# Performance work log

Hardware: AMD Instinct MI355X
Metric: run time of the kernel (lower is better)

The kernel has to match this reference:

```python
import jax, jax.numpy as jnp
import numpy as np

# --- physics constants (from source) ---
T_STALL = 5.4 * (1.0 / 100.0)
W_FREE = 1620.0 * (1.0 / 60.0) * 2.0 * np.pi
L_X = 0.129907
L_Y = 0.095724
A = L_X + L_Y
R = 4 * 0.0254
MASS = 6.0
INERTIA = MASS
MOMENT_OF_INERTIA = MASS * (12 * 0.0254) ** 2 / 6.0

LV2WV = np.array([[1, -1, -A], [1, 1, A], [1, 1, -A], [1, -1, A]], dtype=np.float32) / R  # [4,3]
CD2MD = np.array([[1, -1, -1], [1, 1, 1], [1, 1, -1], [1, -1, 1]], dtype=np.float32)      # [4,3]
WT2LA = (LV2WV.T / np.array([INERTIA, INERTIA, MOMENT_OF_INERTIA], dtype=np.float32)[:, None]).astype(np.float32)  # [3,4]

BATCH = 4_000_000


def _rot(c, s):
    # builds [..., 3, 3] = [[c,-s,0],[s,c,0],[0,0,1]]
    z = jnp.zeros_like(c)
    o = jnp.ones_like(c)
    return jnp.stack([
        jnp.stack([c, -s, z], axis=-1),
        jnp.stack([s, c, z], axis=-1),
        jnp.stack([z, z, o], axis=-1),
    ], axis=-2)


def setup_inputs() -> dict:
    key = jax.random.key(0)
    k1, k2 = jax.random.split(key)
    state = jax.random.normal(k1, (BATCH, 6), dtype=jnp.float32)
    control_duty = jax.random.normal(k2, (3,), dtype=jnp.float32)
    t = jnp.zeros((1,), dtype=jnp.float32)
    return {"t": t, "state": state, "control_duty": control_duty}


def reference(t, state, control_duty):
    lv2wv = jnp.asarray(LV2WV)
    cd2md = jnp.asarray(CD2MD)
    wt2la = jnp.asarray(WT2LA)

    absolute_vel = state[..., 3:]            # [..., 3]
    theta = state[..., 2]                    # [...]

    # absolute -> local frame
    a2l = _rot(jnp.cos(-theta), jnp.sin(-theta))                      # [...,3,3]
    local_vel = jnp.einsum('...ij,...j->...i', a2l, absolute_vel)     # [...,3]
    wheel_vel = jnp.einsum('ij,...j->...i', lv2wv, local_vel)         # [...,4]

    motor_duty = cd2md @ control_duty                                 # [4]
    is_same_direction = (jnp.sign(motor_duty * wheel_vel) + 1.0) / 2.0
    wheel_torque = T_STALL * (1.0 - jnp.abs(wheel_vel) * is_same_direction / W_FREE) * motor_duty  # [...,4]

    local_accel = jnp.einsum('ij,...j->...i', wt2la, wheel_torque)    # [...,3]

    # local -> absolute frame
    l2a = _rot(jnp.cos(theta), jnp.sin(theta))
    absolute_accel = jnp.einsum('...ij,...j->...i', l2a, local_accel)

    return jnp.concatenate([absolute_vel, absolute_accel], axis=-1)   # [...,6]
```

## Files before the change

### kernel.cpp

```cpp
#include <hip/hip_runtime.h>
#include <math.h>

namespace k {
constexpr double dA     = 0.129907 + 0.095724;
constexpr double dR     = 4.0 * 0.0254;
constexpr double dI     = 6.0;
constexpr double dMOI   = 6.0 * (12.0 * 0.0254) * (12.0 * 0.0254) / 6.0;
constexpr float T_STALL   = (float)(5.4 / 100.0);
constexpr float INV_WFREE = (float)(1.0 / (1620.0 / 60.0 * 2.0 * 3.14159265358979323846));
constexpr float A         = (float)dA;
constexpr float INV_R     = (float)(1.0 / dR);
constexpr float INV_RI    = (float)(1.0 / (dR * dI));
constexpr float A_RMOI    = (float)(dA / (dR * dMOI));
}

__device__ __forceinline__ float wheel_torque(float w, float m) {
    float p = m * w;
    float sgn = (float)(p > 0.0f) - (float)(p < 0.0f);
    float isd = 0.5f * (sgn + 1.0f);
    return k::T_STALL * (1.0f - fabsf(w) * isd * k::INV_WFREE) * m;
}

__device__ __forceinline__ void mecanum_elem(const float st[6],
                                             float m0, float m1, float m2, float m3,
                                             float o[6]) {
    float theta = st[2];
    float s, c;
    sincosf(theta, &s, &c);

    float v0 = st[3], v1 = st[4], v2 = st[5];

    float lv0 = c * v0 + s * v1;
    float lv1 = c * v1 - s * v0;
    float lv2 = v2;

    float al2 = k::A * lv2;
    float w0 = (lv0 - lv1 - al2) * k::INV_R;
    float w1 = (lv0 + lv1 + al2) * k::INV_R;
    float w2 = (lv0 + lv1 - al2) * k::INV_R;
    float w3 = (lv0 - lv1 + al2) * k::INV_R;

    float t0 = wheel_torque(w0, m0);
    float t1 = wheel_torque(w1, m1);
    float t2 = wheel_torque(w2, m2);
    float t3 = wheel_torque(w3, m3);

    float la0 = (t0 + t1 + t2 + t3) * k::INV_RI;
    float la1 = (-t0 + t1 + t2 - t3) * k::INV_RI;
    float la2 = (-t0 + t1 - t2 + t3) * k::A_RMOI;

    float aa0 = c * la0 - s * la1;
    float aa1 = s * la0 + c * la1;

    o[0] = v0; o[1] = v1; o[2] = v2;
    o[3] = aa0; o[4] = aa1; o[5] = la2;
}

__global__ __launch_bounds__(256) void mecanum_pair_kernel(
    const float4* __restrict__ state4,
    const float* __restrict__ cd,
    float4* __restrict__ out4,
    int n_pairs) {
    int i = blockIdx.x * blockDim.x + threadIdx.x;
    if (i >= n_pairs) return;

    float u0 = cd[0], u1 = cd[1], u2 = cd[2];
    float m0 = u0 - u1 - u2;
    float m1 = u0 + u1 + u2;
    float m2 = u0 + u1 - u2;
    float m3 = u0 - u1 + u2;

    float4 a = state4[3 * i + 0];
    float4 b = state4[3 * i + 1];
    float4 g = state4[3 * i + 2];

    float stA[6] = { a.x, a.y, a.z, a.w, b.x, b.y };
    float stB[6] = { b.z, b.w, g.x, g.y, g.z, g.w };
    float oA[6], oB[6];
    mecanum_elem(stA, m0, m1, m2, m3, oA);
    mecanum_elem(stB, m0, m1, m2, m3, oB);

    float4 r0 = { oA[0], oA[1], oA[2], oA[3] };
    float4 r1 = { oA[4], oA[5], oB[0], oB[1] };
    float4 r2 = { oB[2], oB[3], oB[4], oB[5] };
    out4[3 * i + 0] = r0;
    out4[3 * i + 1] = r1;
    out4[3 * i + 2] = r2;
}

__global__ void mecanum_tail_kernel(const float* __restrict__ state,
                                    const float* __restrict__ cd,
                                    float* __restrict__ out,
                                    int start, int n) {
    int i = start + blockIdx.x * blockDim.x + threadIdx.x;
    if (i >= n) return;
    float u0 = cd[0], u1 = cd[1], u2 = cd[2];
    float m0 = u0 - u1 - u2;
    float m1 = u0 + u1 + u2;
    float m2 = u0 + u1 - u2;
    float m3 = u0 - u1 + u2;
    float st[6], o[6];
#pragma unroll
    for (int j = 0; j < 6; ++j) st[j] = state[6 * i + j];
    mecanum_elem(st, m0, m1, m2, m3, o);
#pragma unroll
    for (int j = 0; j < 6; ++j) out[6 * i + j] = o[j];
}

extern "C" void kernel_launch(void* const* d_in, const int* in_sizes, int n_in,
                              void* d_out, int out_size, void* d_ws, size_t ws_size,
                              hipStream_t stream) {
    const float* state = (const float*)d_in[1];
    const float* cd    = (const float*)d_in[2];
    float* out         = (float*)d_out;

    int n = in_sizes[1] / 6;
    int n_pairs = n / 2;

    if (n_pairs > 0) {
        int block = 256;
        int grid = (n_pairs + block - 1) / block;
        mecanum_pair_kernel<<<grid, block, 0, stream>>>(
            (const float4*)state, cd, (float4*)out, n_pairs);
    }
    if (n & 1) {
        mecanum_tail_kernel<<<1, 64, 0, stream>>>(state, cd, out, 2 * n_pairs, n);
    }
}
```

Before: 180.7 us.

## Stage state loads and output stores through LDS for fully coalesced access

```diff
diff --git a/kernel.cpp b/kernel.cpp
--- a/kernel.cpp
+++ b/kernel.cpp
@@ -32,9 +32,8 @@
 
     float lv0 = c * v0 + s * v1;
     float lv1 = c * v1 - s * v0;
-    float lv2 = v2;
 
-    float al2 = k::A * lv2;
+    float al2 = k::A * v2;
     float w0 = (lv0 - lv1 - al2) * k::INV_R;
     float w1 = (lv0 + lv1 + al2) * k::INV_R;
     float w2 = (lv0 + lv1 - al2) * k::INV_R;
@@ -52,17 +51,31 @@
     float aa0 = c * la0 - s * la1;
     float aa1 = s * la0 + c * la1;
 
-    o[0] = v0; o[1] = v1; o[2] = v2;
+    o[0] = st[3]; o[1] = st[4]; o[2] = st[5];
     o[3] = aa0; o[4] = aa1; o[5] = la2;
 }
 
-__global__ __launch_bounds__(256) void mecanum_pair_kernel(
+#define PAIRS_PER_BLOCK 256
+#define F4_PER_BLOCK    (PAIRS_PER_BLOCK * 3)
+
+__global__ __launch_bounds__(256) void mecanum_lds_kernel(
     const float4* __restrict__ state4,
     const float* __restrict__ cd,
     float4* __restrict__ out4,
     int n_pairs) {
-    int i = blockIdx.x * blockDim.x + threadIdx.x;
-    if (i >= n_pairs) return;
+    __shared__ float4 s_in[F4_PER_BLOCK];
+    __shared__ float4 s_out[F4_PER_BLOCK];
+
+    const int tid = threadIdx.x;
+    const int pair_base = blockIdx.x * PAIRS_PER_BLOCK;
+    const int f4_base = pair_base * 3;
+    const int total4 = n_pairs * 3;
+
+#pragma unroll
+    for (int j = 0; j < 3; ++j) {
+        int g = f4_base + j * 256 + tid;
+        if (g < total4) s_in[j * 256 + tid] = state4[g];
+    }
 
     float u0 = cd[0], u1 = cd[1], u2 = cd[2];
     float m0 = u0 - u1 - u2;
@@ -70,22 +83,31 @@
     float m2 = u0 + u1 - u2;
     float m3 = u0 - u1 + u2;
 
-    float4 a = state4[3 * i + 0];
-    float4 b = state4[3 * i + 1];
-    float4 g = state4[3 * i + 2];
+    __syncthreads();
 
-    float stA[6] = { a.x, a.y, a.z, a.w, b.x, b.y };
-    float stB[6] = { b.z, b.w, g.x, g.y, g.z, g.w };
-    float oA[6], oB[6];
-    mecanum_elem(stA, m0, m1, m2, m3, oA);
-    mecanum_elem(stB, m0, m1, m2, m3, oB);
+    if (pair_base + tid < n_pairs) {
+        float4 a = s_in[3 * tid + 0];
+        float4 b = s_in[3 * tid + 1];
+        float4 g = s_in[3 * tid + 2];
 
-    float4 r0 = { oA[0], oA[1], oA[2], oA[3] };
-    float4 r1 = { oA[4], oA[5], oB[0], oB[1] };
-    float4 r2 = { oB[2], oB[3], oB[4], oB[5] };
-    out4[3 * i + 0] = r0;
-    out4[3 * i + 1] = r1;
-    out4[3 * i + 2] = r2;
+        float stA[6] = { a.x, a.y, a.z, a.w, b.x, b.y };
+        float stB[6] = { b.z, b.w, g.x, g.y, g.z, g.w };
+        float oA[6], oB[6];
+        mecanum_elem(stA, m0, m1, m2, m3, oA);
+        mecanum_elem(stB, m0, m1, m2, m3, oB);
+
+        s_out[3 * tid + 0] = make_float4(oA[0], oA[1], oA[2], oA[3]);
+        s_out[3 * tid + 1] = make_float4(oA[4], oA[5], oB[0], oB[1]);
+        s_out[3 * tid + 2] = make_float4(oB[2], oB[3], oB[4], oB[5]);
+    }
+
+    __syncthreads();
+
+#pragma unroll
+    for (int j = 0; j < 3; ++j) {
+        int g = f4_base + j * 256 + tid;
+        if (g < total4) out4[g] = s_out[j * 256 + tid];
+    }
 }
 
 __global__ void mecanum_tail_kernel(const float* __restrict__ state,
@@ -118,9 +140,8 @@
     int n_pairs = n / 2;
 
     if (n_pairs > 0) {
-        int block = 256;
-        int grid = (n_pairs + block - 1) / block;
-        mecanum_pair_kernel<<<grid, block, 0, stream>>>(
+        int grid = (n_pairs + PAIRS_PER_BLOCK - 1) / PAIRS_PER_BLOCK;
+        mecanum_lds_kernel<<<grid, 256, 0, stream>>>(
             (const float4*)state, cd, (float4*)out, n_pairs);
     }
     if (n & 1) {
```

Measured after the change: 174.8 us. -3.3%, faster.

## Process eight elements per thread and use fast sin/cos intrinsics

Applied to the files above, without the earlier changes.

```diff
diff --git a/kernel.cpp b/kernel.cpp
--- a/kernel.cpp
+++ b/kernel.cpp
@@ -25,16 +25,15 @@
                                              float m0, float m1, float m2, float m3,
                                              float o[6]) {
     float theta = st[2];
-    float s, c;
-    sincosf(theta, &s, &c);
+    float s = __sinf(theta);
+    float c = __cosf(theta);
 
     float v0 = st[3], v1 = st[4], v2 = st[5];
 
     float lv0 = c * v0 + s * v1;
     float lv1 = c * v1 - s * v0;
-    float lv2 = v2;
 
-    float al2 = k::A * lv2;
+    float al2 = k::A * v2;
     float w0 = (lv0 - lv1 - al2) * k::INV_R;
     float w1 = (lv0 + lv1 + al2) * k::INV_R;
     float w2 = (lv0 + lv1 - al2) * k::INV_R;
@@ -56,36 +55,49 @@
     o[3] = aa0; o[4] = aa1; o[5] = la2;
 }
 
-__global__ __launch_bounds__(256) void mecanum_pair_kernel(
-    const float4* __restrict__ state4,
+__global__ __launch_bounds__(256, 4) void mecanum_ilp_kernel(
+    const float4* __restrict__ in4,
     const float* __restrict__ cd,
     float4* __restrict__ out4,
-    int n_pairs) {
+    int n_groups) {
     int i = blockIdx.x * blockDim.x + threadIdx.x;
-    if (i >= n_pairs) return;
+    if (i >= n_groups) return;
+
+    const int base = i * 12;
+
+    float4 v[12];
+#pragma unroll
+    for (int j = 0; j < 12; ++j) v[j] = in4[base + j];
 
     float u0 = cd[0], u1 = cd[1], u2 = cd[2];
-    float m0 = u0 - u1 - u2;
-    float m1 = u0 + u1 + u2;
-    float m2 = u0 + u1 - u2;
-    float m3 = u0 - u1 + u2;
+    const float m0 = u0 - u1 - u2;
+    const float m1 = u0 + u1 + u2;
+    const float m2 = u0 + u1 - u2;
+    const float m3 = u0 - u1 + u2;
 
-    float4 a = state4[3 * i + 0];
-    float4 b = state4[3 * i + 1];
-    float4 g = state4[3 * i + 2];
+    float r[48];
+#pragma unroll
+    for (int j = 0; j < 12; ++j) {
+        r[4 * j + 0] = v[j].x;
+        r[4 * j + 1] = v[j].y;
+        r[4 * j + 2] = v[j].z;
+        r[4 * j + 3] = v[j].w;
+    }
 
-    float stA[6] = { a.x, a.y, a.z, a.w, b.x, b.y };
-    float stB[6] = { b.z, b.w, g.x, g.y, g.z, g.w };
-    float oA[6], oB[6];
-    mecanum_elem(stA, m0, m1, m2, m3, oA);
-    mecanum_elem(stB, m0, m1, m2, m3, oB);
+#pragma unroll
+    for (int e = 0; e < 8; ++e) {
+        float st[6], o[6];
+#pragma unroll
+        for (int q = 0; q < 6; ++q) st[q] = r[6 * e + q];
+        mecanum_elem(st, m0, m1, m2, m3, o);
+#pragma unroll
+        for (int q = 0; q < 6; ++q) r[6 * e + q] = o[q];
+    }
 
-    float4 r0 = { oA[0], oA[1], oA[2], oA[3] };
-    float4 r1 = { oA[4], oA[5], oB[0], oB[1] };
-    float4 r2 = { oB[2], oB[3], oB[4], oB[5] };
-    out4[3 * i + 0] = r0;
-    out4[3 * i + 1] = r1;
-    out4[3 * i + 2] = r2;
+#pragma unroll
+    for (int j = 0; j < 12; ++j)
+        out4[base + j] = make_float4(r[4 * j + 0], r[4 * j + 1],
+                                     r[4 * j + 2], r[4 * j + 3]);
 }
 
 __global__ void mecanum_tail_kernel(const float* __restrict__ state,
@@ -115,15 +127,15 @@
     float* out         = (float*)d_out;
 
     int n = in_sizes[1] / 6;
-    int n_pairs = n / 2;
+    int n_groups = n / 8;
 
-    if (n_pairs > 0) {
-        int block = 256;
-        int grid = (n_pairs + block - 1) / block;
-        mecanum_pair_kernel<<<grid, block, 0, stream>>>(
-            (const float4*)state, cd, (float4*)out, n_pairs);
+    if (n_groups > 0) {
+        int grid = (n_groups + 255) / 256;
+        mecanum_ilp_kernel<<<grid, 256, 0, stream>>>(
+            (const float4*)state, cd, (float4*)out, n_groups);
     }
-    if (n & 1) {
-        mecanum_tail_kernel<<<1, 64, 0, stream>>>(state, cd, out, 2 * n_pairs, n);
+    int done = n_groups * 8;
+    if (done < n) {
+        mecanum_tail_kernel<<<1, 64, 0, stream>>>(state, cd, out, done, n);
     }
 }
```

Result: slower. 225.9 us (+25.0%).
